# Optimization experiments

Hardware: AMD Instinct MI355X
Metric: run time of the kernel (lower is better)

Reference implementation:

```python
import jax, jax.numpy as jnp
from jax import lax
import numpy as np

B0 = 2          # batch
S = 32          # spatial grid side; L = S*S + 2
L = S * S + 2
DM = 256        # d_model
ED = 512        # d_inner = expand_factor * d_model
N = 16          # d_state
R = 16          # dt_rank = ceil(d_model/16)
K = 4           # d_conv


def _dwconv(x, w, b):
    # x: (B, L, ED) -> causal depthwise conv1d, kernel K, left-pad K-1 (== torch pad K-1 then [:, :, :L])
    xt = jnp.transpose(x, (0, 2, 1))  # (B, ED, L)
    o = lax.conv_general_dilated(xt, w, (1,), [(K - 1, 0)],
                                 feature_group_count=ED,
                                 dimension_numbers=('NCH', 'OIH', 'NCH'))
    return jnp.transpose(o + b[None, :, None], (0, 2, 1))


def _ssm(x, Alog, Dp, xp_w, dt_w, dt_b):
    # x: (B, L, ED); selective scan (mamba.py math, pscan=True path)
    A = -jnp.exp(Alog)                       # (ED, N)
    dBC = x @ xp_w.T                          # (B, L, R+2N)
    delta = jax.nn.softplus(dBC[..., :R] @ dt_w.T + dt_b)  # (B, L, ED)
    Bm = dBC[..., R:R + N]                    # (B, L, N)
    Cm = dBC[..., R + N:]                     # (B, L, N)
    dA = jnp.exp(delta[..., None] * A)        # (B, L, ED, N)
    dBx = (delta * x)[..., None] * Bm[:, :, None, :]  # (B, L, ED, N)

    def comb(e1, e2):
        a1, b1 = e1
        a2, b2 = e2
        return a1 * a2, a2 * b1 + b2

    _, hs = lax.associative_scan(comb, (dA, dBx), axis=1)  # h_t = dA_t*h_{t-1} + dBx_t
    return jnp.einsum('blen,bln->ble', hs, Cm) + Dp * x


def _cross(t):
    # keep first/last token, transpose the SxS interior grid (row-major <-> col-major)
    b, l, d = t.shape
    inner = t[:, 1:-1].reshape(b, S, S, d).transpose(0, 2, 1, 3).reshape(b, S * S, d)
    return jnp.concatenate([t[:, :1], inner, t[:, -1:]], axis=1)


def _branch(xz, cw, cb, xp, dw, db, Al, Dp):
    xa, za = jnp.split(xz, 2, axis=-1)
    xa = jax.nn.silu(_dwconv(xa, cw, cb))
    return _ssm(xa, Al, Dp, xp, dw, db) * jax.nn.silu(za)


def _forward(x, in_w, out_w, *p):
    xz = x @ in_w.T  # (B, L, 2*ED)
    (cwa, cba, xpa, dwa, dba, Ala, Da,
     cwb, cbb, xpb, dwb, dbb, Alb, Db,
     cwc, cbc, xpc, dwc, dbc, Alc, Dc,
     cwd, cbd, xpd, dwd, dbd, Ald, Dd) = p
    ga = _branch(xz, cwa, cba, xpa, dwa, dba, Ala, Da)                # forward scan
    gb = _branch(xz[:, ::-1], cwb, cbb, xpb, dwb, dbb, Alb, Db)       # reversed scan
    xzc = _cross(xz)
    gc = _branch(xzc, cwc, cbc, xpc, dwc, dbc, Alc, Dc)               # transposed scan
    gd = _branch(xzc[:, ::-1], cwd, cbd, xpd, dwd, dbd, Ald, Dd)      # reversed-transposed scan
    # gating commutes with token permutations, so reassemble gated outputs
    y = (ga + gb[:, ::-1] + _cross(gc) + _cross(gd)[:, ::-1]) * 0.25  # divide_output=True
    return y @ out_w.T


def setup_inputs() -> dict:
    keys = jax.random.split(jax.random.key(0), 64)
    it = iter(keys)

    def nrm(shape, scale=0.02):
        return scale * jax.random.normal(next(it), shape, dtype=jnp.float32)

    d = {}
    d['x'] = jax.random.normal(next(it), (B0, L, DM), dtype=jnp.float32)
    d['in_w'] = nrm((2 * ED, DM))
    d['out_w'] = nrm((DM, ED))
    std = R ** -0.5
    for s in ['a', 'b', 'c', 'd']:
        d[f'conv_w_{s}'] = nrm((ED, 1, K), 0.1)
        d[f'conv_b_{s}'] = jnp.zeros((ED,), jnp.float32)
        d[f'xp_w_{s}'] = nrm((R + 2 * N, ED))
        d[f'dt_w_{s}'] = jax.random.uniform(next(it), (ED, R), minval=-std, maxval=std, dtype=jnp.float32)
        dt = jnp.exp(jax.random.uniform(next(it), (ED,), dtype=jnp.float32)
                     * (np.float32(np.log(0.1)) - np.float32(np.log(0.001))) + np.float32(np.log(0.001)))
        d[f'dt_b_{s}'] = dt + jnp.log(-jnp.expm1(-dt))  # inverse-softplus init
        d[f'Alog_{s}'] = jnp.log(jnp.tile(jnp.arange(1, N + 1, dtype=jnp.float32), (ED, 1)))
        d[f'D_{s}'] = jnp.ones((ED,), jnp.float32)
    return d


def reference(x, in_w, out_w,
              conv_w_a, conv_b_a, xp_w_a, dt_w_a, dt_b_a, Alog_a, D_a,
              conv_w_b, conv_b_b, xp_w_b, dt_w_b, dt_b_b, Alog_b, D_b,
              conv_w_c, conv_b_c, xp_w_c, dt_w_c, dt_b_c, Alog_c, D_c,
              conv_w_d, conv_b_d, xp_w_d, dt_w_d, dt_b_d, Alog_d, D_d):
    return _forward(x, in_w, out_w,
                    conv_w_a, conv_b_a, xp_w_a, dt_w_a, dt_b_a, Alog_a, D_a,
                    conv_w_b, conv_b_b, xp_w_b, dt_w_b, dt_b_b, Alog_b, D_b,
                    conv_w_c, conv_b_c, xp_w_c, dt_w_c, dt_b_c, Alog_c, D_c,
                    conv_w_d, conv_b_d, xp_w_d, dt_w_d, dt_b_d, Alog_d, D_d)
```

## Files before the change

### kernel.cpp

```cpp
#include <hip/hip_runtime.h>
#include <math.h>

#define LL 1026
#define EDim 512
#define MM 2052
#define NC 8
#define LC 128

struct Params {
  const float* cw[4];
  const float* cb[4];
  const float* xpw[4];
  const float* dtw[4];
  const float* dtb[4];
  const float* Al[4];
  const float* Dp[4];
};

__device__ __forceinline__ int sigma_map(int branch, int l) {
  if (branch & 1) l = LL - 1 - l;
  if (branch & 2) {
    if (l > 0 && l < LL - 1) {
      int p = l - 1;
      l = 1 + ((p & 31) << 5) + (p >> 5);
    }
  }
  return l;
}

__device__ __forceinline__ float silu_f(float v) { return v / (1.f + expf(-v)); }

template<int CTRL>
__device__ __forceinline__ float dpp_mov0(float x) {
  int r = __builtin_amdgcn_update_dpp(0, __float_as_int(x), CTRL, 0xF, 0xF, false);
  return __int_as_float(r);
}

__global__ __launch_bounds__(256) void k1_gemm_in(
    const float* __restrict__ x, const float* __restrict__ w,
    float* __restrict__ xa, float* __restrict__ sz) {
  __shared__ float As[32][65];
  __shared__ float Bs[32][65];
  const int t = threadIdx.x;
  const int tx = t & 15, ty = t >> 4;
  const int m0 = blockIdx.x * 64, n0 = blockIdx.y * 64;
  float acc[4][4] = {};
  for (int k0 = 0; k0 < 256; k0 += 32) {
    #pragma unroll
    for (int p = 0; p < 2; ++p) {
      int f = t + p * 256;
      int row = f >> 3, cf = f & 7;
      int gr = m0 + row; gr = gr < MM ? gr : MM - 1;
      float4 v = *(const float4*)(x + (size_t)gr * 256 + k0 + cf * 4);
      As[cf*4+0][row] = v.x; As[cf*4+1][row] = v.y;
      As[cf*4+2][row] = v.z; As[cf*4+3][row] = v.w;
      int gn = n0 + row;
      float4 u = *(const float4*)(w + (size_t)gn * 256 + k0 + cf * 4);
      Bs[cf*4+0][row] = u.x; Bs[cf*4+1][row] = u.y;
      Bs[cf*4+2][row] = u.z; Bs[cf*4+3][row] = u.w;
    }
    __syncthreads();
    #pragma unroll
    for (int k = 0; k < 32; ++k) {
      float a0 = As[k][ty*4+0], a1 = As[k][ty*4+1], a2 = As[k][ty*4+2], a3 = As[k][ty*4+3];
      float b0 = Bs[k][tx*4+0], b1 = Bs[k][tx*4+1], b2 = Bs[k][tx*4+2], b3 = Bs[k][tx*4+3];
      acc[0][0]=fmaf(a0,b0,acc[0][0]); acc[0][1]=fmaf(a0,b1,acc[0][1]); acc[0][2]=fmaf(a0,b2,acc[0][2]); acc[0][3]=fmaf(a0,b3,acc[0][3]);
      acc[1][0]=fmaf(a1,b0,acc[1][0]); acc[1][1]=fmaf(a1,b1,acc[1][1]); acc[1][2]=fmaf(a1,b2,acc[1][2]); acc[1][3]=fmaf(a1,b3,acc[1][3]);
      acc[2][0]=fmaf(a2,b0,acc[2][0]); acc[2][1]=fmaf(a2,b1,acc[2][1]); acc[2][2]=fmaf(a2,b2,acc[2][2]); acc[2][3]=fmaf(a2,b3,acc[2][3]);
      acc[3][0]=fmaf(a3,b0,acc[3][0]); acc[3][1]=fmaf(a3,b1,acc[3][1]); acc[3][2]=fmaf(a3,b2,acc[3][2]); acc[3][3]=fmaf(a3,b3,acc[3][3]);
    }
    __syncthreads();
  }
  #pragma unroll
  for (int i = 0; i < 4; ++i) {
    int gm = m0 + ty*4 + i;
    if (gm < MM) {
      #pragma unroll
      for (int j = 0; j < 4; ++j) {
        int gn = n0 + tx*4 + j;
        float v = acc[i][j];
        if (gn < 512) xa[(size_t)gm*512 + gn] = v;
        else          sz[(size_t)gm*512 + gn - 512] = silu_f(v);
      }
    }
  }
}

__global__ __launch_bounds__(256) void k2_branch(
    Params P, const float* __restrict__ xa,
    float* __restrict__ xac, float* __restrict__ delta, float* __restrict__ bcg) {
  __shared__ float xcS[16][516];
  __shared__ float dBCs[16][49];
  const int t = threadIdx.x;
  const int l0 = blockIdx.x * 16;
  const int b  = blockIdx.y;
  const int br = blockIdx.z;
  const int e0 = 2 * t;
  const float* cw = P.cw[br];
  const float w00 = cw[e0*4+0], w01 = cw[e0*4+1], w02 = cw[e0*4+2], w03 = cw[e0*4+3];
  const float w10 = cw[(e0+1)*4+0], w11 = cw[(e0+1)*4+1], w12 = cw[(e0+1)*4+2], w13 = cw[(e0+1)*4+3];
  const float cb0 = P.cb[br][e0], cb1 = P.cb[br][e0+1];
  const float* xab = xa + (size_t)b * LL * 512;
  const size_t obase = (size_t)(br*2 + b) * LL;

  float h0x=0,h0y=0,h1x=0,h1y=0,h2x=0,h2y=0,h3x=0,h3y=0;
  for (int i = -3; i < 16; ++i) {
    int l = l0 + i;
    float cx = 0.f, cy = 0.f;
    if (l >= 0 && l < LL) {
      int pos = sigma_map(br, l);
      float2 v = *(const float2*)(xab + (size_t)pos * 512 + e0);
      cx = v.x; cy = v.y;
    }
    h0x=h1x; h0y=h1y; h1x=h2x; h1y=h2y; h2x=h3x; h2y=h3y; h3x=cx; h3y=cy;
    if (i >= 0) {
      float o0 = fmaf(w00,h0x, fmaf(w01,h1x, fmaf(w02,h2x, fmaf(w03,h3x, cb0))));
      float o1 = fmaf(w10,h0y, fmaf(w11,h1y, fmaf(w12,h2y, fmaf(w13,h3y, cb1))));
      o0 = silu_f(o0); o1 = silu_f(o1);
      *(float2*)&xcS[i][e0] = make_float2(o0, o1);
      if (l < LL)
        *(float2*)(xac + (obase + l) * 512 + e0) = make_float2(o0, o1);
    }
  }
  __syncthreads();

  const int rowi = t & 15;
  const int r0 = t >> 4;
  const float* xpw = P.xpw[br];
  const float4* xr4 = (const float4*)&xcS[rowi][0];
  const float4* wa = (const float4*)(xpw + (size_t)r0 * 512);
  const float4* wb = (const float4*)(xpw + (size_t)(r0 + 16) * 512);
  const float4* wc = (const float4*)(xpw + (size_t)(r0 + 32) * 512);
  float acc0 = 0.f, acc1 = 0.f, acc2 = 0.f;
  #pragma unroll 8
  for (int e4 = 0; e4 < 128; ++e4) {
    float4 xv = xr4[e4];
    float4 a = wa[e4], bb = wb[e4], c = wc[e4];
    acc0 = fmaf(xv.x,a.x, fmaf(xv.y,a.y, fmaf(xv.z,a.z, fmaf(xv.w,a.w, acc0))));
    acc1 = fmaf(xv.x,bb.x,fmaf(xv.y,bb.y,fmaf(xv.z,bb.z,fmaf(xv.w,bb.w,acc1))));
    acc2 = fmaf(xv.x,c.x, fmaf(xv.y,c.y, fmaf(xv.z,c.z, fmaf(xv.w,c.w, acc2))));
  }
  dBCs[rowi][r0]      = acc0;
  dBCs[rowi][r0 + 16] = acc1;
  dBCs[rowi][r0 + 32] = acc2;
  __syncthreads();

  for (int idx = t; idx < 512; idx += 256) {
    int row = idx >> 5, c = idx & 31;
    int l = l0 + row;
    if (l < LL) bcg[(obase + l)*32 + c] = dBCs[row][16 + c];
  }

  const float* dtw = P.dtw[br];
  float dw0[16], dw1[16];
  #pragma unroll
  for (int r = 0; r < 16; ++r) { dw0[r] = dtw[e0*16 + r]; dw1[r] = dtw[(e0+1)*16 + r]; }
  const float db0 = P.dtb[br][e0], db1 = P.dtb[br][e0+1];
  for (int row = 0; row < 16; ++row) {
    int l = l0 + row;
    if (l >= LL) break;
    float s0 = db0, s1 = db1;
    #pragma unroll
    for (int r = 0; r < 16; ++r) {
      float d = dBCs[row][r];
      s0 = fmaf(d, dw0[r], s0);
      s1 = fmaf(d, dw1[r], s1);
    }
    float sp0 = fmaxf(s0, 0.f) + log1pf(expf(-fabsf(s0)));
    float sp1 = fmaxf(s1, 0.f) + log1pf(expf(-fabsf(s1)));
    *(float2*)(delta + (obase + l)*512 + e0) = make_float2(sp0, sp1);
  }
}

__global__ __launch_bounds__(256) void k3a_chunk(
    Params P, const float* __restrict__ xac, const float* __restrict__ delta,
    const float* __restrict__ bcg, float* __restrict__ Pc, float* __restrict__ Qc) {
  __shared__ float dT[16][33], xT[16][33], bT[16][33];
  const int t = threadIdx.x;
  const int eL = t >> 4, n = t & 15;
  const int e0 = blockIdx.x * 16;
  const int b = blockIdx.y;
  const int br = blockIdx.z / NC, c = blockIdx.z % NC;
  const size_t sbase = (size_t)(br*2 + b) * LL;
  const float* dl = delta + sbase * 512;
  const float* xc = xac + sbase * 512;
  const float* bc = bcg + sbase * 32;
  const float A_en = -expf(P.Al[br][(e0 + eL)*16 + n]);
  const int l0 = c * LC;
  const int lend = (c == NC-1) ? LL : (l0 + LC);
  float h = 0.f, dsum = 0.f;

  for (int c0 = l0; c0 < lend; c0 += 32) {
    #pragma unroll
    for (int p = 0; p < 2; ++p) {
      int idx = t + p*256;
      int s = idx >> 4, ee = idx & 15;
      int l = c0 + s;
      float dv = 0.f, xv = 0.f, bv = 0.f;
      if (l < lend) {
        dv = dl[(size_t)l*512 + e0 + ee];
        xv = xc[(size_t)l*512 + e0 + ee];
        bv = bc[l*32 + ee];
      }
      dT[ee][s] = dv; xT[ee][s] = xv; bT[ee][s] = bv;
    }
    __syncthreads();
    float da[32], dbx[32];
    #pragma unroll
    for (int s = 0; s < 32; ++s) {
      float d = dT[eL][s];
      da[s]  = __expf(d * A_en);
      dbx[s] = d * xT[eL][s] * bT[n][s];
      dsum += d;
    }
    #pragma unroll
    for (int s = 0; s < 32; ++s) h = fmaf(da[s], h, dbx[s]);
    __syncthreads();
  }
  size_t oi = ((((size_t)(br*2 + b)*NC + c)*32 + blockIdx.x)*256 + t);
  Pc[oi] = __expf(dsum * A_en);
  Qc[oi] = h;
}

__global__ __launch_bounds__(256) void k3b_scan(
    Params P, const float* __restrict__ xac, const float* __restrict__ delta,
    const float* __restrict__ bcg, const float* __restrict__ sz,
    const float* __restrict__ Pc, const float* __restrict__ Qc,
    float* __restrict__ g) {
  __shared__ float dT[16][33], xT[16][33], bT[16][33], cT[16][33];
  __shared__ float ybuf[32][17];
  const int t = threadIdx.x;
  const int eL = t >> 4, n = t & 15;
  const int e0 = blockIdx.x * 16;
  const int b = blockIdx.y;
  const int br = blockIdx.z / NC, c = blockIdx.z % NC;
  const size_t sbase = (size_t)(br*2 + b) * LL;
  const float* dl = delta + sbase * 512;
  const float* xc = xac + sbase * 512;
  const float* bc = bcg + sbase * 32;
  const float A_en = -expf(P.Al[br][(e0 + eL)*16 + n]);
  const float Dval = P.Dp[br][e0 + (t & 15)];
  const float* szb = sz + (size_t)b * LL * 512;
  float* gb = g + (size_t)br * MM * 512 + (size_t)b * LL * 512;

  float h = 0.f;
  for (int cc = 0; cc < c; ++cc) {
    size_t ii = ((((size_t)(br*2 + b)*NC + cc)*32 + blockIdx.x)*256 + t);
    h = fmaf(Pc[ii], h, Qc[ii]);
  }

  const int l0c = c * LC;
  const int lend = (c == NC-1) ? LL : (l0c + LC);
  for (int c0 = l0c; c0 < lend; c0 += 32) {
    #pragma unroll
    for (int p = 0; p < 2; ++p) {
      int idx = t + p*256;
      int s = idx >> 4, ee = idx & 15;
      int l = c0 + s;
      float dv = 0.f, xv = 0.f, bv = 0.f, cv = 0.f;
      if (l < lend) {
        dv = dl[(size_t)l*512 + e0 + ee];
        xv = xc[(size_t)l*512 + e0 + ee];
        bv = bc[l*32 + ee];
        cv = bc[l*32 + 16 + ee];
      }
      dT[ee][s] = dv; xT[ee][s] = xv; bT[ee][s] = bv; cT[ee][s] = cv;
    }
    __syncthreads();

    float da[32], dbx[32], ccv[32];
    #pragma unroll
    for (int s = 0; s < 32; ++s) {
      float d  = dT[eL][s];
      float xv = xT[eL][s];
      da[s]  = __expf(d * A_en);
      dbx[s] = d * xv * bT[n][s];
      ccv[s] = cT[n][s];
    }
    #pragma unroll
    for (int s = 0; s < 32; ++s) {
      h = fmaf(da[s], h, dbx[s]);
      float r = h * ccv[s];
      r += dpp_mov0<0xB1>(r);
      r += dpp_mov0<0x4E>(r);
      r += dpp_mov0<0x114>(r);
      r += dpp_mov0<0x118>(r);
      if (n == 15) ybuf[s][eL] = r;
    }
    __syncthreads();

    #pragma unroll
    for (int p = 0; p < 2; ++p) {
      int idx = t + p*256;
      int s = idx >> 4, ee = idx & 15;
      int l = c0 + s;
      if (l < lend) {
        float yv = fmaf(Dval, xT[ee][s], ybuf[s][ee]);
        int pos = sigma_map(br, l);
        float szv = szb[(size_t)pos * 512 + e0 + ee];
        gb[(size_t)pos * 512 + e0 + ee] = yv * szv;
      }
    }
    __syncthreads();
  }
}

__global__ __launch_bounds__(256) void k4_gemm_out(
    const float* __restrict__ g, const float* __restrict__ w, float* __restrict__ out) {
  __shared__ float As[32][65];
  __shared__ float Bs[32][33];
  const int t = threadIdx.x;
  const int tx = t & 15, ty = t >> 4;
  const int m0 = blockIdx.x * 64, n0 = blockIdx.y * 32;
  const float* g1 = g + (size_t)MM*512;
  const float* g2 = g + (size_t)2*MM*512;
  const float* g3 = g + (size_t)3*MM*512;
  float acc[4][2] = {};
  for (int k0 = 0; k0 < 512; k0 += 32) {
    #pragma unroll
    for (int p = 0; p < 8; ++p) {
      int idx = t + p*256;
      int row = idx >> 5, kk = idx & 31;
      int gm = m0 + row; gm = gm < MM ? gm : MM - 1;
      size_t ga = (size_t)gm*512 + k0 + kk;
      As[kk][row] = 0.25f * (g[ga] + g1[ga] + g2[ga] + g3[ga]);
    }
    #pragma unroll
    for (int p = 0; p < 4; ++p) {
      int idx = t + p*256;
      int row = idx >> 5, kk = idx & 31;
      Bs[kk][row] = w[(size_t)(n0 + row)*512 + k0 + kk];
    }
    __syncthreads();
    #pragma unroll
    for (int k = 0; k < 32; ++k) {
      float a0 = As[k][ty*4+0], a1 = As[k][ty*4+1], a2 = As[k][ty*4+2], a3 = As[k][ty*4+3];
      float b0 = Bs[k][tx*2+0], b1 = Bs[k][tx*2+1];
      acc[0][0]=fmaf(a0,b0,acc[0][0]); acc[0][1]=fmaf(a0,b1,acc[0][1]);
      acc[1][0]=fmaf(a1,b0,acc[1][0]); acc[1][1]=fmaf(a1,b1,acc[1][1]);
      acc[2][0]=fmaf(a2,b0,acc[2][0]); acc[2][1]=fmaf(a2,b1,acc[2][1]);
      acc[3][0]=fmaf(a3,b0,acc[3][0]); acc[3][1]=fmaf(a3,b1,acc[3][1]);
    }
    __syncthreads();
  }
  #pragma unroll
  for (int i = 0; i < 4; ++i) {
    int gm = m0 + ty*4 + i;
    if (gm < MM) {
      out[(size_t)gm*256 + n0 + tx*2 + 0] = acc[i][0];
      out[(size_t)gm*256 + n0 + tx*2 + 1] = acc[i][1];
    }
  }
}

extern "C" void kernel_launch(void* const* d_in, const int* in_sizes, int n_in,
                              void* d_out, int out_size, void* d_ws, size_t ws_size,
                              hipStream_t stream) {
  const float* x    = (const float*)d_in[0];
  const float* in_w = (const float*)d_in[1];
  const float* out_w= (const float*)d_in[2];
  Params prm;
  for (int s = 0; s < 4; ++s) {
    prm.cw[s]  = (const float*)d_in[3 + s*7 + 0];
    prm.cb[s]  = (const float*)d_in[3 + s*7 + 1];
    prm.xpw[s] = (const float*)d_in[3 + s*7 + 2];
    prm.dtw[s] = (const float*)d_in[3 + s*7 + 3];
    prm.dtb[s] = (const float*)d_in[3 + s*7 + 4];
    prm.Al[s]  = (const float*)d_in[3 + s*7 + 5];
    prm.Dp[s]  = (const float*)d_in[3 + s*7 + 6];
  }
  float* ws = (float*)d_ws;
  const size_t SZ1 = (size_t)MM * 512;
  float* xa   = ws;
  float* szp  = ws + SZ1;
  float* xac  = ws + 2*SZ1;
  float* dlt  = ws + 6*SZ1;
  float* bc   = ws + 10*SZ1;
  float* gbuf = ws + 10*SZ1 + (size_t)4*MM*32;
  float* Pc = xa;
  float* Qc = xa + (size_t)8*NC*32*256;

  k1_gemm_in<<<dim3(33, 16), 256, 0, stream>>>(x, in_w, xa, szp);
  k2_branch <<<dim3(65, 2, 4), 256, 0, stream>>>(prm, xa, xac, dlt, bc);
  k3a_chunk <<<dim3(32, 2, 4*NC), 256, 0, stream>>>(prm, xac, dlt, bc, Pc, Qc);
  k3b_scan  <<<dim3(32, 2, 4*NC), 256, 0, stream>>>(prm, xac, dlt, bc, szp, Pc, Qc, gbuf);
  k4_gemm_out<<<dim3(33, 8), 256, 0, stream>>>(gbuf, out_w, (float*)d_out);
}
```

Baseline: 330.5 us.

## Accumulate branch outputs atomically, use fast math, vectorize LDS reads, retile output GEMM

The four branch scans now atomically add their scaled gated outputs into one shared accumulator, which k2 zeroes beforehand. This replaces four separate g buffers that the output GEMM had to read and average. The change also switches SiLU, softplus and exp to fast intrinsics, vectorizes LDS reads in both GEMMs with re-padded tiles, and shrinks the output GEMM tile to 32x32 for more blocks. It trades four-buffer traffic for atomic contention and a zeroing pass, and fast math loosens accuracy slightly.

```diff
diff --git a/kernel.cpp b/kernel.cpp
--- a/kernel.cpp
+++ b/kernel.cpp
@@ -28,7 +28,12 @@
   return l;
 }
 
-__device__ __forceinline__ float silu_f(float v) { return v / (1.f + expf(-v)); }
+__device__ __forceinline__ float silu_f(float v) {
+  return v * __builtin_amdgcn_rcpf(1.f + __expf(-v));
+}
+__device__ __forceinline__ float softplus_f(float s) {
+  return fmaxf(s, 0.f) + __logf(1.f + __expf(-fabsf(s)));
+}
 
 template<int CTRL>
 __device__ __forceinline__ float dpp_mov0(float x) {
@@ -39,8 +44,8 @@
 __global__ __launch_bounds__(256) void k1_gemm_in(
     const float* __restrict__ x, const float* __restrict__ w,
     float* __restrict__ xa, float* __restrict__ sz) {
-  __shared__ float As[32][65];
-  __shared__ float Bs[32][65];
+  __shared__ float As[32][68];
+  __shared__ float Bs[32][68];
   const int t = threadIdx.x;
   const int tx = t & 15, ty = t >> 4;
   const int m0 = blockIdx.x * 64, n0 = blockIdx.y * 64;
@@ -62,8 +67,10 @@
     __syncthreads();
     #pragma unroll
     for (int k = 0; k < 32; ++k) {
-      float a0 = As[k][ty*4+0], a1 = As[k][ty*4+1], a2 = As[k][ty*4+2], a3 = As[k][ty*4+3];
-      float b0 = Bs[k][tx*4+0], b1 = Bs[k][tx*4+1], b2 = Bs[k][tx*4+2], b3 = Bs[k][tx*4+3];
+      float4 av = *(const float4*)&As[k][ty*4];
+      float4 bv = *(const float4*)&Bs[k][tx*4];
+      float a0 = av.x, a1 = av.y, a2 = av.z, a3 = av.w;
+      float b0 = bv.x, b1 = bv.y, b2 = bv.z, b3 = bv.w;
       acc[0][0]=fmaf(a0,b0,acc[0][0]); acc[0][1]=fmaf(a0,b1,acc[0][1]); acc[0][2]=fmaf(a0,b2,acc[0][2]); acc[0][3]=fmaf(a0,b3,acc[0][3]);
       acc[1][0]=fmaf(a1,b0,acc[1][0]); acc[1][1]=fmaf(a1,b1,acc[1][1]); acc[1][2]=fmaf(a1,b2,acc[1][2]); acc[1][3]=fmaf(a1,b3,acc[1][3]);
       acc[2][0]=fmaf(a2,b0,acc[2][0]); acc[2][1]=fmaf(a2,b1,acc[2][1]); acc[2][2]=fmaf(a2,b2,acc[2][2]); acc[2][3]=fmaf(a2,b3,acc[2][3]);
@@ -88,7 +95,8 @@
 
 __global__ __launch_bounds__(256) void k2_branch(
     Params P, const float* __restrict__ xa,
-    float* __restrict__ xac, float* __restrict__ delta, float* __restrict__ bcg) {
+    float* __restrict__ xac, float* __restrict__ delta, float* __restrict__ bcg,
+    float* __restrict__ acc_out) {
   __shared__ float xcS[16][516];
   __shared__ float dBCs[16][49];
   const int t = threadIdx.x;
@@ -96,6 +104,13 @@
   const int b  = blockIdx.y;
   const int br = blockIdx.z;
   const int e0 = 2 * t;
+
+  if (br == 0) {
+    float* ab = acc_out + ((size_t)b * LL + l0) * 512;
+    int nmax = (LL - l0 < 16 ? LL - l0 : 16) * 512;
+    for (int idx = t; idx < nmax; idx += 256) ab[idx] = 0.f;
+  }
+
   const float* cw = P.cw[br];
   const float w00 = cw[e0*4+0], w01 = cw[e0*4+1], w02 = cw[e0*4+2], w03 = cw[e0*4+3];
   const float w10 = cw[(e0+1)*4+0], w11 = cw[(e0+1)*4+1], w12 = cw[(e0+1)*4+2], w13 = cw[(e0+1)*4+3];
@@ -166,9 +181,7 @@
       s0 = fmaf(d, dw0[r], s0);
       s1 = fmaf(d, dw1[r], s1);
     }
-    float sp0 = fmaxf(s0, 0.f) + log1pf(expf(-fabsf(s0)));
-    float sp1 = fmaxf(s1, 0.f) + log1pf(expf(-fabsf(s1)));
-    *(float2*)(delta + (obase + l)*512 + e0) = make_float2(sp0, sp1);
+    *(float2*)(delta + (obase + l)*512 + e0) = make_float2(softplus_f(s0), softplus_f(s1));
   }
 }
 
@@ -185,7 +198,7 @@
   const float* dl = delta + sbase * 512;
   const float* xc = xac + sbase * 512;
   const float* bc = bcg + sbase * 32;
-  const float A_en = -expf(P.Al[br][(e0 + eL)*16 + n]);
+  const float A_en = -__expf(P.Al[br][(e0 + eL)*16 + n]);
   const int l0 = c * LC;
   const int lend = (c == NC-1) ? LL : (l0 + LC);
   float h = 0.f, dsum = 0.f;
@@ -226,7 +239,7 @@
     Params P, const float* __restrict__ xac, const float* __restrict__ delta,
     const float* __restrict__ bcg, const float* __restrict__ sz,
     const float* __restrict__ Pc, const float* __restrict__ Qc,
-    float* __restrict__ g) {
+    float* __restrict__ acc_out) {
   __shared__ float dT[16][33], xT[16][33], bT[16][33], cT[16][33];
   __shared__ float ybuf[32][17];
   const int t = threadIdx.x;
@@ -238,10 +251,10 @@
   const float* dl = delta + sbase * 512;
   const float* xc = xac + sbase * 512;
   const float* bc = bcg + sbase * 32;
-  const float A_en = -expf(P.Al[br][(e0 + eL)*16 + n]);
+  const float A_en = -__expf(P.Al[br][(e0 + eL)*16 + n]);
   const float Dval = P.Dp[br][e0 + (t & 15)];
   const float* szb = sz + (size_t)b * LL * 512;
-  float* gb = g + (size_t)br * MM * 512 + (size_t)b * LL * 512;
+  float* ab = acc_out + (size_t)b * LL * 512;
 
   float h = 0.f;
   for (int cc = 0; cc < c; ++cc) {
@@ -298,7 +311,7 @@
         float yv = fmaf(Dval, xT[ee][s], ybuf[s][ee]);
         int pos = sigma_map(br, l);
         float szv = szb[(size_t)pos * 512 + e0 + ee];
-        gb[(size_t)pos * 512 + e0 + ee] = yv * szv;
+        atomicAdd(ab + (size_t)pos * 512 + e0 + ee, 0.25f * yv * szv);
       }
     }
     __syncthreads();
@@ -306,24 +319,21 @@
 }
 
 __global__ __launch_bounds__(256) void k4_gemm_out(
-    const float* __restrict__ g, const float* __restrict__ w, float* __restrict__ out) {
-  __shared__ float As[32][65];
-  __shared__ float Bs[32][33];
+    const float* __restrict__ acc_in, const float* __restrict__ w,
+    float* __restrict__ out) {
+  __shared__ float As[32][38];
+  __shared__ float Bs[32][38];
   const int t = threadIdx.x;
   const int tx = t & 15, ty = t >> 4;
-  const int m0 = blockIdx.x * 64, n0 = blockIdx.y * 32;
-  const float* g1 = g + (size_t)MM*512;
-  const float* g2 = g + (size_t)2*MM*512;
-  const float* g3 = g + (size_t)3*MM*512;
-  float acc[4][2] = {};
+  const int m0 = blockIdx.x * 32, n0 = blockIdx.y * 32;
+  float acc[2][2] = {};
   for (int k0 = 0; k0 < 512; k0 += 32) {
     #pragma unroll
-    for (int p = 0; p < 8; ++p) {
+    for (int p = 0; p < 4; ++p) {
       int idx = t + p*256;
       int row = idx >> 5, kk = idx & 31;
       int gm = m0 + row; gm = gm < MM ? gm : MM - 1;
-      size_t ga = (size_t)gm*512 + k0 + kk;
-      As[kk][row] = 0.25f * (g[ga] + g1[ga] + g2[ga] + g3[ga]);
+      As[kk][row] = acc_in[(size_t)gm*512 + k0 + kk];
     }
     #pragma unroll
     for (int p = 0; p < 4; ++p) {
@@ -334,21 +344,20 @@
     __syncthreads();
     #pragma unroll
     for (int k = 0; k < 32; ++k) {
-      float a0 = As[k][ty*4+0], a1 = As[k][ty*4+1], a2 = As[k][ty*4+2], a3 = As[k][ty*4+3];
-      float b0 = Bs[k][tx*2+0], b1 = Bs[k][tx*2+1];
-      acc[0][0]=fmaf(a0,b0,acc[0][0]); acc[0][1]=fmaf(a0,b1,acc[0][1]);
-      acc[1][0]=fmaf(a1,b0,acc[1][0]); acc[1][1]=fmaf(a1,b1,acc[1][1]);
-      acc[2][0]=fmaf(a2,b0,acc[2][0]); acc[2][1]=fmaf(a2,b1,acc[2][1]);
-      acc[3][0]=fmaf(a3,b0,acc[3][0]); acc[3][1]=fmaf(a3,b1,acc[3][1]);
+      float2 av = *(const float2*)&As[k][ty*2];
+      float2 bv = *(const float2*)&Bs[k][tx*2];
+      acc[0][0]=fmaf(av.x,bv.x,acc[0][0]); acc[0][1]=fmaf(av.x,bv.y,acc[0][1]);
+      acc[1][0]=fmaf(av.y,bv.x,acc[1][0]); acc[1][1]=fmaf(av.y,bv.y,acc[1][1]);
     }
     __syncthreads();
   }
   #pragma unroll
-  for (int i = 0; i < 4; ++i) {
-    int gm = m0 + ty*4 + i;
+  for (int i = 0; i < 2; ++i) {
+    int gm = m0 + ty*2 + i;
     if (gm < MM) {
-      out[(size_t)gm*256 + n0 + tx*2 + 0] = acc[i][0];
-      out[(size_t)gm*256 + n0 + tx*2 + 1] = acc[i][1];
+      #pragma unroll
+      for (int j = 0; j < 2; ++j)
+        out[(size_t)gm*256 + n0 + tx*2 + j] = acc[i][j];
     }
   }
 }
@@ -376,13 +385,13 @@
   float* xac  = ws + 2*SZ1;
   float* dlt  = ws + 6*SZ1;
   float* bc   = ws + 10*SZ1;
-  float* gbuf = ws + 10*SZ1 + (size_t)4*MM*32;
+  float* acc  = ws + 10*SZ1 + (size_t)4*MM*32;
   float* Pc = xa;
   float* Qc = xa + (size_t)8*NC*32*256;
 
   k1_gemm_in<<<dim3(33, 16), 256, 0, stream>>>(x, in_w, xa, szp);
-  k2_branch <<<dim3(65, 2, 4), 256, 0, stream>>>(prm, xa, xac, dlt, bc);
+  k2_branch <<<dim3(65, 2, 4), 256, 0, stream>>>(prm, xa, xac, dlt, bc, acc);
   k3a_chunk <<<dim3(32, 2, 4*NC), 256, 0, stream>>>(prm, xac, dlt, bc, Pc, Qc);
-  k3b_scan  <<<dim3(32, 2, 4*NC), 256, 0, stream>>>(prm, xac, dlt, bc, szp, Pc, Qc, gbuf);
-  k4_gemm_out<<<dim3(33, 8), 256, 0, stream>>>(gbuf, out_w, (float*)d_out);
-}
+  k3b_scan  <<<dim3(32, 2, 4*NC), 256, 0, stream>>>(prm, xac, dlt, bc, szp, Pc, Qc, acc);
+  k4_gemm_out<<<dim3(65, 8), 256, 0, stream>>>(acc, out_w, (float*)d_out);
+}
```

Measured after the change: 300.4 us. -9.1%, faster.
